# Kernel optimization log

Hardware: AMD Instinct MI355X
Metric: run time of the kernel (lower is better)

The kernel has to match this reference:

```python
import jax, jax.numpy as jnp
import numpy as np

B, S, H = 2, 2048, 2048
E, I, TOPK = 8, 1408, 2


def setup_inputs() -> dict:
    key = jax.random.key(0)
    k0, k1, k2, k3, k4 = jax.random.split(key, 5)
    return {
        "hidden_states": jax.random.normal(k0, (B, S, H), dtype=jnp.float32),
        "Wr": jax.random.normal(k1, (H, E), dtype=jnp.float32) * 0.02,
        "Wg": jax.random.normal(k2, (E, H, I), dtype=jnp.float32) * 0.02,
        "Wu": jax.random.normal(k3, (E, H, I), dtype=jnp.float32) * 0.02,
        "Wd": jax.random.normal(k4, (E, I, H), dtype=jnp.float32) * 0.02,
    }


def reference(hidden_states, Wr, Wg, Wu, Wd):
    b, s, h = hidden_states.shape
    x = hidden_states.reshape(-1, h)                      # [T, H]
    T = x.shape[0]
    router_logits = x @ Wr                                # [T, E]
    probs = jax.nn.softmax(router_logits.astype(jnp.float32), axis=-1)
    top_w, top_i = jax.lax.top_k(probs, TOPK)             # [T, k]
    top_w = top_w / jnp.sum(top_w, axis=-1, keepdims=True)  # norm_topk_prob
    top_w = top_w.astype(x.dtype)
    # combine weights per (token, expert): zero where expert not selected
    cw = jnp.zeros((T, E), dtype=x.dtype).at[
        jnp.arange(T)[:, None], top_i].add(top_w)         # [T, E]
    # per-expert SwiGLU MLP computed densely, masked/weighted by cw
    g = jax.nn.silu(jnp.einsum('th,ehi->tei', x, Wg))     # [T, E, I]
    u = jnp.einsum('th,ehi->tei', x, Wu)                  # [T, E, I]
    y = jnp.einsum('tei,eih->teh', g * u, Wd)             # [T, E, H]
    out = jnp.einsum('te,teh->th', cw, y)                 # [T, H]
    return out.reshape(b, s, h), router_logits
```

## Files before the change

kernel.cpp:

```cpp
#include <hip/hip_runtime.h>

#define T_TOK 4096
#define HD 2048
#define NE 8
#define NI 1408

typedef __bf16 bf16x8 __attribute__((ext_vector_type(8)));
typedef float f32x4 __attribute__((ext_vector_type(4)));
typedef unsigned short ushort8 __attribute__((ext_vector_type(8)));

#define S_WAITCNT_VMCNT(n) asm volatile("s_waitcnt vmcnt(" #n ")" ::: "memory")
__device__ __forceinline__ void wave_barrier() {
  asm volatile("" ::: "memory");
  __builtin_amdgcn_s_barrier();
  asm volatile("" ::: "memory");
}

__device__ __forceinline__ unsigned short f2bf(float f) {
  unsigned int u = __float_as_uint(f);
  u += 0x7FFFu + ((u >> 16) & 1u);
  return (unsigned short)(u >> 16);
}
__device__ __forceinline__ float bf2f(unsigned short u) {
  return __uint_as_float((unsigned int)u << 16);
}

__device__ __forceinline__ void gload_lds16(const void* g, void* l) {
  __builtin_amdgcn_global_load_lds(
      (const __attribute__((address_space(1))) unsigned int*)g,
      (__attribute__((address_space(3))) unsigned int*)l, 16, 0, 0);
}

__device__ __forceinline__ void transpose_body_nt(const float* s,
                                                  unsigned short* d,
                                                  int R, int C, int r0, int c0) {
  int tid = threadIdx.x;
  int rg = tid & 7, cg = tid >> 3;
  const float* sb = s + (size_t)(r0 + rg * 8) * C + c0 + cg * 4;
  f32x4 v[8];
#pragma unroll
  for (int j = 0; j < 8; j++)
    v[j] = __builtin_nontemporal_load((const f32x4*)(sb + (size_t)j * C));
  unsigned short* db = d + (size_t)(c0 + cg * 4) * R + r0 + rg * 8;
#pragma unroll
  for (int cc = 0; cc < 4; cc++) {
    ushort8 o;
#pragma unroll
    for (int j = 0; j < 8; j++) o[j] = f2bf(v[j][cc]);
    __builtin_nontemporal_store(o, (ushort8*)(db + (size_t)cc * R));
  }
}

__global__ void prepass_kernel(const float* __restrict__ x,
                               const float* __restrict__ Wr,
                               const float* __restrict__ Wg,
                               const float* __restrict__ Wu,
                               float* __restrict__ logits,
                               unsigned short* __restrict__ xbf,
                               unsigned short* __restrict__ Wgt,
                               unsigned short* __restrict__ Wut,
                               int4* __restrict__ tokinfo,
                               int* __restrict__ cnt) {
  const int bid = blockIdx.x;
  if (bid < 704) {
    int q = bid;
    int xt = q % 11; q /= 11;
    int rs = q & 3;  q >>= 2;
    int e = q >> 1, sel = q & 1;
    const float* sp = (sel ? Wu : Wg) + (size_t)e * HD * NI;
    unsigned short* dp = (sel ? Wut : Wgt) + (size_t)e * HD * NI;
#pragma unroll
    for (int rt = 0; rt < 8; rt++)
      transpose_body_nt(sp, dp, HD, NI, (rs * 8 + rt) * 64, xt * 128);
  } else {
    int wv = threadIdx.x >> 6, lane = threadIdx.x & 63;
    int t = (bid - 704) * 4 + wv;
    const float* xr = x + (size_t)t * HD;
    unsigned short* xbr = xbf + (size_t)t * HD;
    float acc[NE];
#pragma unroll
    for (int e = 0; e < NE; e++) acc[e] = 0.f;
    for (int hi = 0; hi < HD / 256; hi++) {
      int h = hi * 256 + lane * 4;
      f32x4 xv = __builtin_nontemporal_load((const f32x4*)(xr + h));
      ushort4 o = { f2bf(xv[0]), f2bf(xv[1]), f2bf(xv[2]), f2bf(xv[3]) };
      *(ushort4*)(xbr + h) = o;
#pragma unroll
      for (int j = 0; j < 4; j++) {
        const float4* w4 = (const float4*)(Wr + (size_t)(h + j) * NE);
        float4 a = w4[0], b = w4[1];
        float xs = xv[j];
        acc[0] += xs * a.x; acc[1] += xs * a.y; acc[2] += xs * a.z; acc[3] += xs * a.w;
        acc[4] += xs * b.x; acc[5] += xs * b.y; acc[6] += xs * b.z; acc[7] += xs * b.w;
      }
    }
#pragma unroll
    for (int m = 32; m > 0; m >>= 1) {
#pragma unroll
      for (int e = 0; e < NE; e++) acc[e] += __shfl_xor(acc[e], m, 64);
    }
    if (lane < NE) logits[(size_t)t * NE + lane] = acc[lane];
    if (lane == 0) {
      int e0 = 0;
#pragma unroll
      for (int e = 1; e < NE; e++) if (acc[e] > acc[e0]) e0 = e;
      int e1 = (e0 == 0) ? 1 : 0;
#pragma unroll
      for (int e = 0; e < NE; e++) if (e != e0 && acc[e] > acc[e1]) e1 = e;
      float ex = expf(acc[e1] - acc[e0]);
      float w0 = 1.f / (1.f + ex);
      float w1 = ex / (1.f + ex);
      atomicAdd(&cnt[e0], 1);
      atomicAdd(&cnt[e1], 1);
      tokinfo[t] = make_int4(e0, e1, __float_as_int(w0), __float_as_int(w1));
    }
  }
}

__global__ void route_finalize_kernel(const int4* __restrict__ tokinfo,
                                      int* __restrict__ cnt,
                                      int* __restrict__ row_tok,
                                      int2* __restrict__ tok2row) {
  if (threadIdx.x == 0) {
    int o = 0;
    for (int e = 0; e < NE; e++) { cnt[8 + e] = o; o += cnt[e]; }
  }
  __syncthreads();
  for (int t = threadIdx.x; t < T_TOK; t += 1024) {
    int4 info = tokinfo[t];
    int p0 = atomicAdd(&cnt[16 + info.x], 1);
    int r0 = cnt[8 + info.x] + p0;
    row_tok[r0] = t;
    int p1 = atomicAdd(&cnt[16 + info.y], 1);
    int r1 = cnt[8 + info.y] + p1;
    row_tok[r1] = t;
    tok2row[t] = make_int2(r0, r1);
  }
}

__launch_bounds__(256, 2)
__global__ void gemm1_kernel(const unsigned short* __restrict__ xbf,
                             const unsigned short* __restrict__ Wgt,
                             const unsigned short* __restrict__ Wut,
                             const float* __restrict__ Wd,
                             unsigned short* __restrict__ Wdt,
                             unsigned short* __restrict__ act,
                             const int* __restrict__ row_tok,
                             const int* __restrict__ cnt) {
  const int F = blockIdx.x + 11 * (blockIdx.y + 32 * blockIdx.z);
  const int e = F & 7;
  const int r = F >> 3;
  if (r >= 352) {
    const int t = r - 352;
    const int xt = t / 22, yt = t % 22;
    transpose_body_nt(Wd + (size_t)e * NI * HD, Wdt + (size_t)e * NI * HD,
                      NI, HD, yt * 64, xt * 128);
    return;
  }
  const int nt = r >> 5;
  const int mt = r & 31;
  const int c = cnt[e];
  if (mt * 128 >= c) return;
  const int off = cnt[8 + e];
  const int rowbase = off + mt * 128, rowend = off + c;
  const int i0 = nt * 128;
  __shared__ __align__(16) char smem[73728];
  const int lane = threadIdx.x & 63, w = threadIdx.x >> 6;
  const int wr = w >> 1, wc = w & 1;

  const int rr0 = w * 16 + (lane >> 2);
  const int rr1 = rr0 + 64;
  const int q0 = (lane & 3) ^ ((rr0 >> 1) & 3);
  const int q1 = (lane & 3) ^ ((rr1 >> 1) & 3);
  int g0 = rowbase + rr0; if (g0 > rowend - 1) g0 = rowend - 1;
  int g1 = rowbase + rr1; if (g1 > rowend - 1) g1 = rowend - 1;
  const size_t tokA0 = (size_t)row_tok[g0] * HD;
  const size_t tokA1 = (size_t)row_tok[g1] * HD;
  const size_t bB0 = ((size_t)e * NI + i0 + rr0) * HD;
  const size_t bB1 = ((size_t)e * NI + i0 + rr1) * HD;
  const int ldsA = w * 1024;

  f32x4 zero = {0.f, 0.f, 0.f, 0.f};
  f32x4 accg[4][4], accu[4][4];
#pragma unroll
  for (int a = 0; a < 4; a++)
#pragma unroll
    for (int b = 0; b < 4; b++) { accg[a][b] = zero; accu[a][b] = zero; }

  auto stage = [&](int buf, int ks) {
    const int k0 = ks * 32;
    char* base = smem + buf * 24576;
    gload_lds16(xbf + tokA0 + k0 + q0 * 8, base + ldsA);
    gload_lds16(xbf + tokA1 + k0 + q1 * 8, base + ldsA + 4096);
    gload_lds16(Wgt + bB0 + k0 + q0 * 8, base + 8192 + ldsA);
    gload_lds16(Wgt + bB1 + k0 + q1 * 8, base + 8192 + ldsA + 4096);
    gload_lds16(Wut + bB0 + k0 + q0 * 8, base + 16384 + ldsA);
    gload_lds16(Wut + bB1 + k0 + q1 * 8, base + 16384 + ldsA + 4096);
  };
  const int rl = lane & 15, kslot = lane >> 4;
  auto compute = [&](int buf) {
    const char* base = smem + buf * 24576;
    bf16x8 af[4], bg[4], bu[4];
#pragma unroll
    for (int mi = 0; mi < 4; mi++) {
      int rr = wr * 64 + mi * 16 + rl;
      int byt = rr * 64 + ((kslot ^ ((rr >> 1) & 3)) << 4);
      af[mi] = *(const bf16x8*)(base + byt);
    }
#pragma unroll
    for (int ni = 0; ni < 4; ni++) {
      int rr = wc * 64 + ni * 16 + rl;
      int byt = rr * 64 + ((kslot ^ ((rr >> 1) & 3)) << 4);
      bg[ni] = *(const bf16x8*)(base + 8192 + byt);
      bu[ni] = *(const bf16x8*)(base + 16384 + byt);
    }
    __builtin_amdgcn_s_setprio(1);
#pragma unroll
    for (int mi = 0; mi < 4; mi++)
#pragma unroll
      for (int ni = 0; ni < 4; ni++) {
        accg[mi][ni] = __builtin_amdgcn_mfma_f32_16x16x32_bf16(af[mi], bg[ni], accg[mi][ni], 0, 0, 0);
        accu[mi][ni] = __builtin_amdgcn_mfma_f32_16x16x32_bf16(af[mi], bu[ni], accu[mi][ni], 0, 0, 0);
      }
    __builtin_amdgcn_s_setprio(0);
  };

  stage(0, 0);
  stage(1, 1);
  const int NKS = HD / 32;
  for (int ks = 0; ks < NKS; ks++) {
    if (ks < NKS - 1) {
      S_WAITCNT_VMCNT(6);
    } else {
      S_WAITCNT_VMCNT(0);
    }
    wave_barrier();
    if (ks + 2 < NKS) stage((ks + 2) % 3, ks + 2);
    compute(ks % 3);
  }

  const int rh = lane >> 4;
#pragma unroll
  for (int mi = 0; mi < 4; mi++)
#pragma unroll
    for (int ni = 0; ni < 4; ni++)
#pragma unroll
      for (int j = 0; j < 4; j++) {
        int grow = rowbase + wr * 64 + mi * 16 + rh * 4 + j;
        if (grow < rowend) {
          int gcol = i0 + wc * 64 + ni * 16 + rl;
          float g = accg[mi][ni][j], u = accu[mi][ni][j];
          float val = g / (1.f + __expf(-g)) * u;
          act[(size_t)grow * NI + gcol] = f2bf(val);
        }
      }
}

__launch_bounds__(256, 3)
__global__ void gemm2_kernel(const unsigned short* __restrict__ act,
                             const unsigned short* __restrict__ Wdt,
                             unsigned short* __restrict__ y,
                             const int* __restrict__ cnt) {
  const int f = blockIdx.x + 16 * (blockIdx.y + 32 * blockIdx.z);
  const int e = f & 7;
  const int rem = f >> 3;
  const int nt = rem >> 5;
  const int mt = rem & 31;
  const int c = cnt[e];
  if (mt * 128 >= c) return;
  const int off = cnt[8 + e];
  const int rowbase = off + mt * 128, rowend = off + c;
  const int n0 = nt * 128;
  __shared__ __align__(16) char smem[49152];
  const int lane = threadIdx.x & 63, w = threadIdx.x >> 6;
  const int wr = w >> 1, wc = w & 1;

  const int rr0 = w * 16 + (lane >> 2);
  const int rr1 = rr0 + 64;
  const int q0 = (lane & 3) ^ ((rr0 >> 1) & 3);
  const int q1 = (lane & 3) ^ ((rr1 >> 1) & 3);
  int g0 = rowbase + rr0; if (g0 > rowend - 1) g0 = rowend - 1;
  int g1 = rowbase + rr1; if (g1 > rowend - 1) g1 = rowend - 1;
  const size_t aA0 = (size_t)g0 * NI;
  const size_t aA1 = (size_t)g1 * NI;
  const size_t bB0 = ((size_t)e * HD + n0 + rr0) * NI;
  const size_t bB1 = ((size_t)e * HD + n0 + rr1) * NI;
  const int ldsA = w * 1024;

  f32x4 zero = {0.f, 0.f, 0.f, 0.f};
  f32x4 acc[4][4];
#pragma unroll
  for (int a = 0; a < 4; a++)
#pragma unroll
    for (int b = 0; b < 4; b++) acc[a][b] = zero;

  auto stage = [&](int buf, int ks) {
    const int k0 = ks * 32;
    char* base = smem + buf * 16384;
    gload_lds16(act + aA0 + k0 + q0 * 8, base + ldsA);
    gload_lds16(act + aA1 + k0 + q1 * 8, base + ldsA + 4096);
    gload_lds16(Wdt + bB0 + k0 + q0 * 8, base + 8192 + ldsA);
    gload_lds16(Wdt + bB1 + k0 + q1 * 8, base + 8192 + ldsA + 4096);
  };
  const int rl = lane & 15, kslot = lane >> 4;
  auto compute = [&](int buf) {
    const char* base = smem + buf * 16384;
    bf16x8 af[4], bf[4];
#pragma unroll
    for (int mi = 0; mi < 4; mi++) {
      int rr = wr * 64 + mi * 16 + rl;
      int byt = rr * 64 + ((kslot ^ ((rr >> 1) & 3)) << 4);
      af[mi] = *(const bf16x8*)(base + byt);
    }
#pragma unroll
    for (int ni = 0; ni < 4; ni++) {
      int rr = wc * 64 + ni * 16 + rl;
      int byt = rr * 64 + ((kslot ^ ((rr >> 1) & 3)) << 4);
      bf[ni] = *(const bf16x8*)(base + 8192 + byt);
    }
    __builtin_amdgcn_s_setprio(1);
#pragma unroll
    for (int mi = 0; mi < 4; mi++)
#pragma unroll
      for (int ni = 0; ni < 4; ni++)
        acc[mi][ni] = __builtin_amdgcn_mfma_f32_16x16x32_bf16(af[mi], bf[ni], acc[mi][ni], 0, 0, 0);
    __builtin_amdgcn_s_setprio(0);
  };

  stage(0, 0);
  stage(1, 1);
  const int NKS = NI / 32;
  for (int ks = 0; ks < NKS; ks++) {
    if (ks < NKS - 1) {
      S_WAITCNT_VMCNT(4);
    } else {
      S_WAITCNT_VMCNT(0);
    }
    wave_barrier();
    if (ks + 2 < NKS) stage((ks + 2) % 3, ks + 2);
    compute(ks % 3);
  }

  const int rh = lane >> 4;
#pragma unroll
  for (int mi = 0; mi < 4; mi++)
#pragma unroll
    for (int ni = 0; ni < 4; ni++)
#pragma unroll
      for (int j = 0; j < 4; j++) {
        int grow = rowbase + wr * 64 + mi * 16 + rh * 4 + j;
        if (grow < rowend) {
          int gcol = n0 + wc * 64 + ni * 16 + rl;
          y[(size_t)grow * HD + gcol] = f2bf(acc[mi][ni][j]);
        }
      }
}

__global__ void combine_kernel(const unsigned short* __restrict__ y,
                               const int2* __restrict__ tok2row,
                               const int4* __restrict__ tokinfo,
                               float* __restrict__ out) {
  int t = blockIdx.x, tid = threadIdx.x;
  int2 rr = tok2row[t];
  int4 info = tokinfo[t];
  float w0 = __int_as_float(info.z), w1 = __int_as_float(info.w);
  ushort8 a = ((const ushort8*)(y + (size_t)rr.x * HD))[tid];
  ushort8 b = ((const ushort8*)(y + (size_t)rr.y * HD))[tid];
  float4 o0, o1;
  o0.x = w0 * bf2f(a[0]) + w1 * bf2f(b[0]);
  o0.y = w0 * bf2f(a[1]) + w1 * bf2f(b[1]);
  o0.z = w0 * bf2f(a[2]) + w1 * bf2f(b[2]);
  o0.w = w0 * bf2f(a[3]) + w1 * bf2f(b[3]);
  o1.x = w0 * bf2f(a[4]) + w1 * bf2f(b[4]);
  o1.y = w0 * bf2f(a[5]) + w1 * bf2f(b[5]);
  o1.z = w0 * bf2f(a[6]) + w1 * bf2f(b[6]);
  o1.w = w0 * bf2f(a[7]) + w1 * bf2f(b[7]);
  float4* op = (float4*)(out + (size_t)t * HD + tid * 8);
  op[0] = o0; op[1] = o1;
}

extern "C" void kernel_launch(void* const* d_in, const int* in_sizes, int n_in,
                              void* d_out, int out_size, void* d_ws, size_t ws_size,
                              hipStream_t stream) {
  const float* x  = (const float*)d_in[0];
  const float* Wr = (const float*)d_in[1];
  const float* Wg = (const float*)d_in[2];
  const float* Wu = (const float*)d_in[3];
  const float* Wd = (const float*)d_in[4];
  float* out = (float*)d_out;
  char* ws = (char*)d_ws;

  unsigned short* xbf = (unsigned short*)(ws);
  unsigned short* Wgt = (unsigned short*)(ws + 16777216);
  unsigned short* Wut = (unsigned short*)(ws + 62914560);
  unsigned short* Wdt = (unsigned short*)(ws + 109051904);
  unsigned short* act = (unsigned short*)(ws + 155189248);
  unsigned short* yb  = (unsigned short*)(ws + 16777216);
  int4*  tokinfo      = (int4*)(ws + 178257920);
  int*   row_tok      = (int*)(ws + 178323456);
  int2*  tok2row      = (int2*)(ws + 178356224);
  int*   cnt          = (int*)(ws + 178388992);

  hipMemsetAsync(cnt, 0, 128, stream);

  prepass_kernel<<<704 + 1024, 256, 0, stream>>>(
      x, Wr, Wg, Wu, out + (size_t)T_TOK * HD, xbf, Wgt, Wut, tokinfo, cnt);
  route_finalize_kernel<<<1, 1024, 0, stream>>>(tokinfo, cnt, row_tok, tok2row);

  gemm1_kernel<<<dim3(11, 32, 16), 256, 0, stream>>>(
      xbf, Wgt, Wut, Wd, Wdt, act, row_tok, cnt);
  gemm2_kernel<<<dim3(16, 32, NE), 256, 0, stream>>>(act, Wdt, yb, cnt);
  combine_kernel<<<T_TOK, 256, 0, stream>>>(yb, tok2row, tokinfo, out);
}
```

Measured before the change: 428.3 us.

## Split gemm1 gate/up across two wave groups with 512-thread blocks

Gemm1 blocks grow from 256 to 512 threads. One half of the waves accumulates the gate projection and the other half the up projection, which halves the per-wave accumulator registers and the B-fragment loads, and each thread now issues three async loads per stage instead of six. The up results are passed through LDS so the gate half can apply SiLU·u and write the activation. The fused Wd transpose branch is reworked so each 512-thread block handles two tiles. This adds two block barriers and an LDS round-trip in the epilogue, and 512-thread blocks with 72KB of LDS may limit how many blocks fit per CU.

```diff
diff --git a/kernel.cpp b/kernel.cpp
--- a/kernel.cpp
+++ b/kernel.cpp
@@ -33,9 +33,9 @@
 
 __device__ __forceinline__ void transpose_body_nt(const float* s,
                                                   unsigned short* d,
-                                                  int R, int C, int r0, int c0) {
-  int tid = threadIdx.x;
-  int rg = tid & 7, cg = tid >> 3;
+                                                  int R, int C, int r0, int c0,
+                                                  int tid256) {
+  int rg = tid256 & 7, cg = tid256 >> 3;
   const float* sb = s + (size_t)(r0 + rg * 8) * C + c0 + cg * 4;
   f32x4 v[8];
 #pragma unroll
@@ -71,7 +71,8 @@
     unsigned short* dp = (sel ? Wut : Wgt) + (size_t)e * HD * NI;
 #pragma unroll
     for (int rt = 0; rt < 8; rt++)
-      transpose_body_nt(sp, dp, HD, NI, (rs * 8 + rt) * 64, xt * 128);
+      transpose_body_nt(sp, dp, HD, NI, (rs * 8 + rt) * 64, xt * 128,
+                        threadIdx.x);
   } else {
     int wv = threadIdx.x >> 6, lane = threadIdx.x & 63;
     int t = (bid - 704) * 4 + wv;
@@ -138,7 +139,7 @@
   }
 }
 
-__launch_bounds__(256, 2)
+__launch_bounds__(512, 4)
 __global__ void gemm1_kernel(const unsigned short* __restrict__ xbf,
                              const unsigned short* __restrict__ Wgt,
                              const unsigned short* __restrict__ Wut,
@@ -151,10 +152,13 @@
   const int e = F & 7;
   const int r = F >> 3;
   if (r >= 352) {
-    const int t = r - 352;
-    const int xt = t / 22, yt = t % 22;
-    transpose_body_nt(Wd + (size_t)e * NI * HD, Wdt + (size_t)e * NI * HD,
-                      NI, HD, yt * 64, xt * 128);
+    if (r < 528) {
+      const int t = r - 352;
+      const int xt = t / 11, ytp = t % 11;
+      const int yt = ytp * 2 + (threadIdx.x >> 8);
+      transpose_body_nt(Wd + (size_t)e * NI * HD, Wdt + (size_t)e * NI * HD,
+                        NI, HD, yt * 64, xt * 128, threadIdx.x & 255);
+    }
     return;
   }
   const int nt = r >> 5;
@@ -166,62 +170,56 @@
   const int i0 = nt * 128;
   __shared__ __align__(16) char smem[73728];
   const int lane = threadIdx.x & 63, w = threadIdx.x >> 6;
-  const int wr = w >> 1, wc = w & 1;
-
-  const int rr0 = w * 16 + (lane >> 2);
-  const int rr1 = rr0 + 64;
-  const int q0 = (lane & 3) ^ ((rr0 >> 1) & 3);
-  const int q1 = (lane & 3) ^ ((rr1 >> 1) & 3);
-  int g0 = rowbase + rr0; if (g0 > rowend - 1) g0 = rowend - 1;
-  int g1 = rowbase + rr1; if (g1 > rowend - 1) g1 = rowend - 1;
-  const size_t tokA0 = (size_t)row_tok[g0] * HD;
-  const size_t tokA1 = (size_t)row_tok[g1] * HD;
-  const size_t bB0 = ((size_t)e * NI + i0 + rr0) * HD;
-  const size_t bB1 = ((size_t)e * NI + i0 + rr1) * HD;
-  const int ldsA = w * 1024;
+  const int half = w >> 2;
+  const int wq = w & 3;
+  const int wr = wq >> 1, wc = wq & 1;
+
+  const int rr = w * 16 + (lane >> 2);
+  const int q = (lane & 3) ^ ((rr >> 1) & 3);
+  int gA = rowbase + rr; if (gA > rowend - 1) gA = rowend - 1;
+  const size_t tokA = (size_t)row_tok[gA] * HD;
+  const size_t bB = ((size_t)e * NI + i0 + rr) * HD;
+  const int ldsW = w * 1024;
 
   f32x4 zero = {0.f, 0.f, 0.f, 0.f};
-  f32x4 accg[4][4], accu[4][4];
+  f32x4 acc[4][4];
 #pragma unroll
   for (int a = 0; a < 4; a++)
 #pragma unroll
-    for (int b = 0; b < 4; b++) { accg[a][b] = zero; accu[a][b] = zero; }
-
+    for (int b = 0; b < 4; b++) acc[a][b] = zero;
+
+  const unsigned short* Wsel = half ? Wut : Wgt;
   auto stage = [&](int buf, int ks) {
     const int k0 = ks * 32;
     char* base = smem + buf * 24576;
-    gload_lds16(xbf + tokA0 + k0 + q0 * 8, base + ldsA);
-    gload_lds16(xbf + tokA1 + k0 + q1 * 8, base + ldsA + 4096);
-    gload_lds16(Wgt + bB0 + k0 + q0 * 8, base + 8192 + ldsA);
-    gload_lds16(Wgt + bB1 + k0 + q1 * 8, base + 8192 + ldsA + 4096);
-    gload_lds16(Wut + bB0 + k0 + q0 * 8, base + 16384 + ldsA);
-    gload_lds16(Wut + bB1 + k0 + q1 * 8, base + 16384 + ldsA + 4096);
+    gload_lds16(xbf + tokA + k0 + q * 8, base + ldsW);
+    gload_lds16(Wgt + bB + k0 + q * 8, base + 8192 + ldsW);
+    gload_lds16(Wut + bB + k0 + q * 8, base + 16384 + ldsW);
   };
   const int rl = lane & 15, kslot = lane >> 4;
+  const int Boff = 8192 + half * 8192;
   auto compute = [&](int buf) {
     const char* base = smem + buf * 24576;
-    bf16x8 af[4], bg[4], bu[4];
+    bf16x8 af[4], bf[4];
 #pragma unroll
     for (int mi = 0; mi < 4; mi++) {
-      int rr = wr * 64 + mi * 16 + rl;
-      int byt = rr * 64 + ((kslot ^ ((rr >> 1) & 3)) << 4);
+      int rw = wr * 64 + mi * 16 + rl;
+      int byt = rw * 64 + ((kslot ^ ((rw >> 1) & 3)) << 4);
       af[mi] = *(const bf16x8*)(base + byt);
     }
 #pragma unroll
     for (int ni = 0; ni < 4; ni++) {
-      int rr = wc * 64 + ni * 16 + rl;
-      int byt = rr * 64 + ((kslot ^ ((rr >> 1) & 3)) << 4);
-      bg[ni] = *(const bf16x8*)(base + 8192 + byt);
-      bu[ni] = *(const bf16x8*)(base + 16384 + byt);
+      int rw = wc * 64 + ni * 16 + rl;
+      int byt = rw * 64 + ((kslot ^ ((rw >> 1) & 3)) << 4);
+      bf[ni] = *(const bf16x8*)(base + Boff + byt);
     }
     __builtin_amdgcn_s_setprio(1);
 #pragma unroll
     for (int mi = 0; mi < 4; mi++)
 #pragma unroll
-      for (int ni = 0; ni < 4; ni++) {
-        accg[mi][ni] = __builtin_amdgcn_mfma_f32_16x16x32_bf16(af[mi], bg[ni], accg[mi][ni], 0, 0, 0);
-        accu[mi][ni] = __builtin_amdgcn_mfma_f32_16x16x32_bf16(af[mi], bu[ni], accu[mi][ni], 0, 0, 0);
-      }
+      for (int ni = 0; ni < 4; ni++)
+        acc[mi][ni] = __builtin_amdgcn_mfma_f32_16x16x32_bf16(
+            af[mi], bf[ni], acc[mi][ni], 0, 0, 0);
     __builtin_amdgcn_s_setprio(0);
   };
 
@@ -230,7 +228,7 @@
   const int NKS = HD / 32;
   for (int ks = 0; ks < NKS; ks++) {
     if (ks < NKS - 1) {
-      S_WAITCNT_VMCNT(6);
+      S_WAITCNT_VMCNT(3);
     } else {
       S_WAITCNT_VMCNT(0);
     }
@@ -239,21 +237,40 @@
     compute(ks % 3);
   }
 
+  __syncthreads();
+  float* uls = (float*)smem;
   const int rh = lane >> 4;
-#pragma unroll
-  for (int mi = 0; mi < 4; mi++)
-#pragma unroll
-    for (int ni = 0; ni < 4; ni++)
-#pragma unroll
-      for (int j = 0; j < 4; j++) {
-        int grow = rowbase + wr * 64 + mi * 16 + rh * 4 + j;
-        if (grow < rowend) {
-          int gcol = i0 + wc * 64 + ni * 16 + rl;
-          float g = accg[mi][ni][j], u = accu[mi][ni][j];
-          float val = g / (1.f + __expf(-g)) * u;
-          act[(size_t)grow * NI + gcol] = f2bf(val);
+  if (half == 1) {
+#pragma unroll
+    for (int mi = 0; mi < 4; mi++)
+#pragma unroll
+      for (int ni = 0; ni < 4; ni++)
+#pragma unroll
+        for (int j = 0; j < 4; j++) {
+          int row = wr * 64 + mi * 16 + rh * 4 + j;
+          int col = wc * 64 + ni * 16 + rl;
+          uls[row * 132 + col] = acc[mi][ni][j];
         }
-      }
+  }
+  __syncthreads();
+  if (half == 0) {
+#pragma unroll
+    for (int mi = 0; mi < 4; mi++)
+#pragma unroll
+      for (int ni = 0; ni < 4; ni++)
+#pragma unroll
+        for (int j = 0; j < 4; j++) {
+          int row = wr * 64 + mi * 16 + rh * 4 + j;
+          int grow = rowbase + row;
+          if (grow < rowend) {
+            int col = wc * 64 + ni * 16 + rl;
+            float g = acc[mi][ni][j];
+            float u = uls[row * 132 + col];
+            float val = g / (1.f + __expf(-g)) * u;
+            act[(size_t)grow * NI + i0 + col] = f2bf(val);
+          }
+        }
+  }
 }
 
 __launch_bounds__(256, 3)
@@ -407,7 +424,7 @@
       x, Wr, Wg, Wu, out + (size_t)T_TOK * HD, xbf, Wgt, Wut, tokinfo, cnt);
   route_finalize_kernel<<<1, 1024, 0, stream>>>(tokinfo, cnt, row_tok, tok2row);
 
-  gemm1_kernel<<<dim3(11, 32, 16), 256, 0, stream>>>(
+  gemm1_kernel<<<dim3(11, 32, 16), 512, 0, stream>>>(
       xbf, Wgt, Wut, Wd, Wdt, act, row_tok, cnt);
   gemm2_kernel<<<dim3(16, 32, NE), 256, 0, stream>>>(act, Wdt, yb, cnt);
   combine_kernel<<<T_TOK, 256, 0, stream>>>(yb, tok2row, tokinfo, out);
```

Result: slower. 457.0 us (+6.7%).
